# Kernel tuning notes

Measured on AMD Instinct MI355X. Metric: run time of the kernel, lower is better.

The kernel has to match this reference:

```python
import jax, jax.numpy as jnp
import numpy as np

B, T, M, E, H, D = 4, 1024, 1024, 1024, 16, 64
SCALE = D ** (-0.5)


def setup_inputs() -> dict:
    key = jax.random.key(0)
    ks = jax.random.split(key, 8)
    w = 0.02  # weight scale for numerical stability of softmax
    return {
        "x": jax.random.normal(ks[0], (B, T, E), jnp.float32),
        "xl_memory": jax.random.normal(ks[1], (B, M, 2, H * D), jnp.float32),
        "relative_positions": jax.random.normal(ks[2], (H, T, M + T), jnp.float32),
        "Wq": jax.random.normal(ks[3], (E, H * D), jnp.float32) * w,
        "bq": jnp.zeros((H * D,), jnp.float32),
        "Wk": jax.random.normal(ks[4], (E, H * D), jnp.float32) * w,
        "bk": jnp.zeros((H * D,), jnp.float32),
        "Wv": jax.random.normal(ks[5], (E, H * D), jnp.float32) * w,
        "bv": jnp.zeros((H * D,), jnp.float32),
        "Wo": jax.random.normal(ks[6], (H * D, E), jnp.float32) * w,
        "bo": jnp.zeros((E,), jnp.float32),
    }


def reference(x, xl_memory, relative_positions, Wq, bq, Wk, bk, Wv, bv, Wo, bo):
    b, t, _ = x.shape
    q = (x @ Wq + bq) * SCALE                     # [b, t, H*D] (scale applied to queries)
    k = x @ Wk + bk
    v = x @ Wv + bv
    k_xl = xl_memory[:, :, 0]                      # [b, m, H*D]
    v_xl = xl_memory[:, :, 1]
    m = k_xl.shape[1]
    keys = jnp.concatenate((k_xl, k), axis=1)      # [b, j, H*D], j = m + t
    values = jnp.concatenate((v_xl, v), axis=1)
    j = keys.shape[1]

    qh = q.reshape(b, t, H, D).transpose(0, 2, 1, 3)       # b h i d
    kh = keys.reshape(b, j, H, D).transpose(0, 2, 1, 3)    # b h j d
    vh = values.reshape(b, j, H, D).transpose(0, 2, 1, 3)  # b h j d

    qk = jnp.einsum("bhid,bhjd->bhij", qh, kh)
    qk = relative_positions[..., -t:, -j:] + qk
    qk = qk * SCALE                                # second scale, faithful to source
    mask = jnp.triu(jnp.ones((t, j), dtype=bool), j - t + 1)
    qk = jnp.where(mask, -jnp.inf, qk)
    attn = jax.nn.softmax(qk, axis=-1)             # dropout p=0.0 -> identity

    qkv = jnp.einsum("bhij,bhjd->bhid", attn, vh)
    qkv = qkv.transpose(0, 2, 1, 3).reshape(b, t, H * D)
    out = qkv @ Wo + bo

    kv_memories = jnp.stack((keys, values), axis=-2)  # [b, j, 2, H*D]
    kv_to_add_xl = kv_memories[:, -m:]                 # [b, m, 2, H*D]
    return out, kv_to_add_xl
```

## Files before the change

### kernel.cpp

```cpp
#include <hip/hip_runtime.h>
#include <hip/hip_bf16.h>

typedef unsigned short u16;
typedef unsigned int u32;
typedef __attribute__((ext_vector_type(8))) short short8;
typedef __attribute__((ext_vector_type(4))) float f32x4;

#define B_ 4
#define T_ 1024
#define E_ 1024
#define NH 16
#define HD 1024
#define JTOT 2048
#define SCALE 0.125f
#define LOG2E 1.44269504f

__device__ __forceinline__ u16 f2b(float f) {
  u32 x = __float_as_uint(f);
  u32 r = (x + 0x7fffu + ((x >> 16) & 1u)) >> 16;
  return (u16)r;
}
__device__ __forceinline__ u16 f2b_fast(float f) {
  return (u16)((__float_as_uint(f) + 0x8000u) >> 16);
}
__device__ __forceinline__ float b2f(u16 b) {
  return __uint_as_float((u32)b << 16);
}
__device__ __forceinline__ float fexp2(float x) {
  float r;
  asm("v_exp_f32 %0, %1" : "=v"(r) : "v"(x));
  return r;
}

__device__ __forceinline__ void gload_lds16(const void* g, void* l) {
  __builtin_amdgcn_global_load_lds((const __attribute__((address_space(1))) u32*)g,
                                   (__attribute__((address_space(3))) u32*)l, 16, 0, 0);
}

__device__ __forceinline__ short8 pack8(float4 f0, float4 f1) {
  short8 o;
  o[0] = (short)f2b(f0.x); o[1] = (short)f2b(f0.y);
  o[2] = (short)f2b(f0.z); o[3] = (short)f2b(f0.w);
  o[4] = (short)f2b(f1.x); o[5] = (short)f2b(f1.y);
  o[6] = (short)f2b(f1.z); o[7] = (short)f2b(f1.w);
  return o;
}

__global__ __launch_bounds__(256) void cvt_bf16(const float* __restrict__ in,
                                                u16* __restrict__ out, int n8) {
  int i = blockIdx.x * 256 + threadIdx.x;
  if (i >= n8) return;
  const float4* p = (const float4*)in + (size_t)i * 2;
  ((short8*)out)[i] = pack8(p[0], p[1]);
}

__global__ __launch_bounds__(256) void cvt_w4T(const float* __restrict__ Wq, const float* __restrict__ Wk,
                                               const float* __restrict__ Wv, const float* __restrict__ Wo,
                                               u16* __restrict__ wqkvT, u16* __restrict__ woT) {
  __shared__ float tile[64][65];
  const float* W;
  u16* WT;
  int z = blockIdx.z;
  if (z == 0) { W = Wq; WT = wqkvT; }
  else if (z == 1) { W = Wk; WT = wqkvT + (size_t)1024 * 1024; }
  else if (z == 2) { W = Wv; WT = wqkvT + (size_t)2048 * 1024; }
  else { W = Wo; WT = woT; }
  int t = threadIdx.x;
  int r0 = blockIdx.y * 64, c0 = blockIdx.x * 64;
#pragma unroll
  for (int i = 0; i < 16; ++i) {
    int r = i * 4 + (t >> 6), c = t & 63;
    tile[r][c] = W[(size_t)(r0 + r) * 1024 + c0 + c];
  }
  __syncthreads();
#pragma unroll
  for (int i = 0; i < 16; ++i) {
    int r = i * 4 + (t >> 6), c = t & 63;
    WT[(size_t)(c0 + r) * 1024 + r0 + c] = f2b(tile[c][r]);
  }
}

__global__ __launch_bounds__(256) void cvt_xl_k(const float* __restrict__ xl, u16* __restrict__ kt) {
  int i = blockIdx.x * 256 + threadIdx.x;
  int hd8 = i & 127, j = (i >> 7) & 1023, b = i >> 17;
  const float4* p = (const float4*)(xl + ((((size_t)b * 1024 + j) * 2 + 0) * 1024 + (size_t)hd8 * 8));
  short8 o = pack8(p[0], p[1]);
  int h = hd8 >> 3, d0 = (hd8 & 7) * 8;
  int jc = j >> 6, jl = j & 63;
  u16* dst = kt + (((size_t)(b * 16 + h) * 32 + jc) * 4096) + jl * 64 + (d0 ^ (((jl >> 2) & 3) << 4));
  *(short8*)dst = o;
}

__global__ __launch_bounds__(256) void cvt_xl_vT(const float* __restrict__ xl, u16* __restrict__ vt) {
  __shared__ u16 Vl[64 * 72];
  int bx = blockIdx.x;
  int jc = bx & 15, h = (bx >> 4) & 15, b = bx >> 8;
  int t = threadIdx.x;
  int j0 = jc * 64;
#pragma unroll
  for (int it = 0; it < 2; ++it) {
    int p = t + 256 * it;
    int j = p >> 3, d8 = p & 7;
    const float4* src = (const float4*)(xl + ((((size_t)b * 1024 + j0 + j) * 2 + 1) * 1024 + h * 64 + (size_t)d8 * 8));
    *(short8*)&Vl[j * 72 + d8 * 8] = pack8(src[0], src[1]);
  }
  __syncthreads();
#pragma unroll
  for (int it = 0; it < 2; ++it) {
    int p = t + 256 * it;
    int d = p >> 3, j8 = p & 7;
    short8 o;
#pragma unroll
    for (int e = 0; e < 8; ++e) o[e] = (short)Vl[(j8 * 8 + e) * 72 + d];
    u16* dst = vt + (((size_t)(b * 16 + h) * 32 + jc) * 4096) + d * 64 + ((j8 * 8) ^ (((d >> 2) & 3) << 4));
    *(short8*)dst = o;
  }
}

__global__ __launch_bounds__(256) void trans_vnew(const u16* __restrict__ vb, u16* __restrict__ vt) {
  __shared__ u16 Vl[64 * 72];
  int bx = blockIdx.x;
  int jcl = bx & 15, h = (bx >> 4) & 15, b = bx >> 8;
  int jc = 16 + jcl;
  int t = threadIdx.x;
  int t0 = jcl * 64;
#pragma unroll
  for (int it = 0; it < 2; ++it) {
    int p = t + 256 * it;
    int j = p >> 3, d8 = p & 7;
    *(short8*)&Vl[j * 72 + d8 * 8] =
        *(const short8*)&vb[((size_t)b * 1024 + t0 + j) * 1024 + h * 64 + d8 * 8];
  }
  __syncthreads();
#pragma unroll
  for (int it = 0; it < 2; ++it) {
    int p = t + 256 * it;
    int d = p >> 3, j8 = p & 7;
    short8 o;
#pragma unroll
    for (int e = 0; e < 8; ++e) o[e] = (short)Vl[(j8 * 8 + e) * 72 + d];
    u16* dst = vt + (((size_t)(b * 16 + h) * 32 + jc) * 4096) + d * 64 + ((j8 * 8) ^ (((d >> 2) & 3) << 4));
    *(short8*)dst = o;
  }
}

__global__ __launch_bounds__(256) void gemm_qkv(
    const u16* __restrict__ A, const u16* __restrict__ BT,
    const float* __restrict__ b0, const float* __restrict__ b1, const float* __restrict__ b2,
    u16* __restrict__ qb, u16* __restrict__ kbp, u16* __restrict__ kt, u16* __restrict__ vb) {
  __shared__ __align__(16) u16 As[128 * 32];
  __shared__ __align__(16) u16 Bs[128 * 32];
  const int t = threadIdx.x;
  const int lane = t & 63, wv = t >> 6;
  const int wr = wv >> 1, wc = wv & 1;
  const int m0 = (blockIdx.x / 24) * 128;
  const int n0 = (blockIdx.x % 24) * 128;
  const int lr = lane & 15, lg = lane >> 4;

  f32x4 acc[4][4] = {};

  for (int kc = 0; kc < 1024; kc += 32) {
    __syncthreads();
#pragma unroll
    for (int i = 0; i < 2; ++i) {
      int p = t + 256 * i;
      gload_lds16(A + (size_t)(m0 + (p >> 2)) * 1024 + kc + (p & 3) * 8, &As[p * 8]);
    }
#pragma unroll
    for (int i = 0; i < 2; ++i) {
      int p = t + 256 * i;
      gload_lds16(BT + (size_t)(n0 + (p >> 2)) * 1024 + kc + (p & 3) * 8, &Bs[p * 8]);
    }
    __syncthreads();

    short8 af[4], bf[4];
#pragma unroll
    for (int mf = 0; mf < 4; ++mf)
      af[mf] = *(const short8*)&As[(wr * 64 + mf * 16 + lr) * 32 + lg * 8];
#pragma unroll
    for (int nf = 0; nf < 4; ++nf)
      bf[nf] = *(const short8*)&Bs[(wc * 64 + nf * 16 + lr) * 32 + lg * 8];
#pragma unroll
    for (int mf = 0; mf < 4; ++mf)
#pragma unroll
      for (int nf = 0; nf < 4; ++nf)
        acc[mf][nf] = __builtin_amdgcn_mfma_f32_16x16x32_bf16(af[mf], bf[nf], acc[mf][nf], 0, 0, 0);
  }

#pragma unroll
  for (int mf = 0; mf < 4; ++mf) {
#pragma unroll
    for (int nf = 0; nf < 4; ++nf) {
#pragma unroll
      for (int r = 0; r < 4; ++r) {
        int row = m0 + wr * 64 + mf * 16 + lg * 4 + r;
        int col = n0 + wc * 64 + nf * 16 + lr;
        float v = acc[mf][nf][r];
        int b = row >> 10, tt = row & 1023;
        if (col < 1024) {
          v += b0[col];
          qb[(size_t)row * HD + col] = f2b(v * (SCALE * SCALE * LOG2E));
        } else if (col < 2048) {
          int hd = col - 1024;
          u16 kv16 = f2b(v + b1[hd]);
          kbp[(size_t)(b * 1024 + tt) * 1024 + hd] = kv16;
          int h = hd >> 6, d = hd & 63, jl = tt & 63, jc = 16 + (tt >> 6);
          kt[(((size_t)(b * 16 + h) * 32 + jc) * 4096) + jl * 64 + (d ^ (((jl >> 2) & 3) << 4))] = kv16;
        } else {
          int hd = col - 2048;
          vb[(size_t)(b * 1024 + tt) * 1024 + hd] = f2b(v + b2[hd]);
        }
      }
    }
  }
}

__global__ __launch_bounds__(256) void kv_expand(const u16* __restrict__ kbp, const u16* __restrict__ vbp,
                                                 float* __restrict__ kvout) {
  int i = blockIdx.x * 256 + threadIdx.x;
  int hd8 = i & 127, tt = (i >> 7) & 1023, b = i >> 17;
  size_t src = ((size_t)(b * 1024 + tt)) * 1024 + (size_t)hd8 * 8;
  short8 k8 = *(const short8*)&kbp[src];
  short8 v8 = *(const short8*)&vbp[src];
  float4 k0, k1, v0, v1;
#pragma unroll
  for (int e = 0; e < 4; ++e) {
    ((float*)&k0)[e] = b2f((u16)k8[e]); ((float*)&k1)[e] = b2f((u16)k8[e + 4]);
    ((float*)&v0)[e] = b2f((u16)v8[e]); ((float*)&v1)[e] = b2f((u16)v8[e + 4]);
  }
  float* kdst = kvout + (((size_t)(b * 1024 + tt) * 2 + 0) * 1024) + hd8 * 8;
  float* vdst = kvout + (((size_t)(b * 1024 + tt) * 2 + 1) * 1024) + hd8 * 8;
  ((float4*)kdst)[0] = k0; ((float4*)kdst)[1] = k1;
  ((float4*)vdst)[0] = v0; ((float4*)vdst)[1] = v1;
}

__global__ __launch_bounds__(256) void gemm_out(
    const u16* __restrict__ A, const u16* __restrict__ BT,
    const float* __restrict__ bias, float* __restrict__ outf) {
  __shared__ __align__(16) u16 As[64 * 32];
  __shared__ __align__(16) u16 Bs[128 * 32];
  const int t = threadIdx.x;
  const int lane = t & 63, wv = t >> 6;
  const int wr = wv >> 1, wc = wv & 1;
  const int m0 = (blockIdx.x >> 3) * 64;
  const int n0 = (blockIdx.x & 7) * 128;
  const int lr = lane & 15, lg = lane >> 4;

  f32x4 acc[2][4] = {};

  for (int kc = 0; kc < 1024; kc += 32) {
    __syncthreads();
    gload_lds16(A + (size_t)(m0 + (t >> 2)) * 1024 + kc + (t & 3) * 8, &As[t * 8]);
#pragma unroll
    for (int i = 0; i < 2; ++i) {
      int p = t + 256 * i;
      gload_lds16(BT + (size_t)(n0 + (p >> 2)) * 1024 + kc + (p & 3) * 8, &Bs[p * 8]);
    }
    __syncthreads();

    short8 af[2], bf[4];
#pragma unroll
    for (int mf = 0; mf < 2; ++mf)
      af[mf] = *(const short8*)&As[(wr * 32 + mf * 16 + lr) * 32 + lg * 8];
#pragma unroll
    for (int nf = 0; nf < 4; ++nf)
      bf[nf] = *(const short8*)&Bs[(wc * 64 + nf * 16 + lr) * 32 + lg * 8];
#pragma unroll
    for (int mf = 0; mf < 2; ++mf)
#pragma unroll
      for (int nf = 0; nf < 4; ++nf)
        acc[mf][nf] = __builtin_amdgcn_mfma_f32_16x16x32_bf16(af[mf], bf[nf], acc[mf][nf], 0, 0, 0);
  }

#pragma unroll
  for (int mf = 0; mf < 2; ++mf)
#pragma unroll
    for (int nf = 0; nf < 4; ++nf)
#pragma unroll
      for (int r = 0; r < 4; ++r) {
        int row = m0 + wr * 32 + mf * 16 + lg * 4 + r;
        int col = n0 + wc * 64 + nf * 16 + lr;
        outf[(size_t)row * E_ + col] = acc[mf][nf][r] + bias[col];
      }
}

__global__ __launch_bounds__(256) void attn_kernel(
    const u16* __restrict__ qb, const u16* __restrict__ kt, const u16* __restrict__ vt,
    const float* __restrict__ rel, u16* __restrict__ aout) {
  __shared__ __align__(16) u16 Ks[2][4096];
  __shared__ __align__(16) u16 Vs[2][4096];
  __shared__ __align__(16) u16 Pl[4096];
  const int bx = blockIdx.x;
  const int b = bx & 3, h = (bx >> 2) & 15, qt = bx >> 6;
  const int i0 = qt * 64;
  const int t = threadIdx.x, lane = t & 63, w = t >> 6;
  const int lr = lane & 15, lg = lane >> 4;
  const int sel = (lr >> 2) & 3;
  const float RC = SCALE * LOG2E;

  const u16* ktb = kt + (size_t)(b * 16 + h) * 32 * 4096;
  const u16* vtb = vt + (size_t)(b * 16 + h) * 32 * 4096;
  const float* relbase = rel + (size_t)h * T_ * JTOT;
  const int ib = i0 + w * 16 + lg * 4;

  short8 qf[2];
#pragma unroll
  for (int kc = 0; kc < 2; ++kc)
    qf[kc] = *(const short8*)&qb[(size_t)(b * T_ + i0 + w * 16 + lr) * HD + h * 64 + kc * 32 + lg * 8];

  short8 vf5;
#pragma unroll
  for (int e = 0; e < 8; ++e) vf5[e] = (lr == 0) ? (short)0x3f80 : (short)0;

  const int nch = qt + 17;

  auto stage = [&](int buf, int jc2) {
    const u16* ksrc = ktb + (size_t)jc2 * 4096;
    const u16* vsrc = vtb + (size_t)jc2 * 4096;
    gload_lds16(ksrc + t * 8, &Ks[buf][t * 8]);
    gload_lds16(ksrc + (t + 256) * 8, &Ks[buf][(t + 256) * 8]);
    gload_lds16(vsrc + t * 8, &Vs[buf][t * 8]);
    gload_lds16(vsrc + (t + 256) * 8, &Vs[buf][(t + 256) * 8]);
  };

  float rl[4][4];
  auto loadrel = [&](int j0) {
#pragma unroll
    for (int nf = 0; nf < 4; ++nf)
#pragma unroll
      for (int r = 0; r < 4; ++r)
        rl[nf][r] = relbase[(size_t)(ib + r) * JTOT + j0 + nf * 16 + lr];
  };

  stage(0, 0);
  asm volatile("" ::: "memory");
  loadrel(0);

  f32x4 o[5] = {};
  float mrow[4];
#pragma unroll
  for (int r = 0; r < 4; ++r) mrow[r] = -__builtin_inff();

  int cur = 0;
  for (int jc = 0; jc < nch; ++jc) {
    asm volatile("s_waitcnt vmcnt(16)" ::: "memory");
    __builtin_amdgcn_sched_barrier(0);
    asm volatile("s_barrier" ::: "memory");
    if (jc + 1 < nch) stage(cur ^ 1, jc + 1);
    asm volatile("" ::: "memory");

    f32x4 s4[4] = {};
    __builtin_amdgcn_s_setprio(1);
#pragma unroll
    for (int nf = 0; nf < 4; ++nf)
#pragma unroll
      for (int kc = 0; kc < 2; ++kc) {
        short8 kf = *(const short8*)&Ks[cur][(nf * 16 + lr) * 64 + ((kc * 32 + lg * 8) ^ (sel << 4))];
        s4[nf] = __builtin_amdgcn_mfma_f32_16x16x32_bf16(qf[kc], kf, s4[nf], 0, 0, 0);
      }
    __builtin_amdgcn_s_setprio(0);

    float p[4][4], lmax[4];
    const bool domask = (jc == qt + 16);
#pragma unroll
    for (int nf = 0; nf < 4; ++nf)
#pragma unroll
      for (int r = 0; r < 4; ++r) {
        float v = fmaf(rl[nf][r], RC, s4[nf][r]);
        if (domask && (nf * 16 + lr) > (w * 16 + lg * 4 + r)) v = -__builtin_inff();
        p[nf][r] = v;
      }
#pragma unroll
    for (int r = 0; r < 4; ++r)
      lmax[r] = fmaxf(fmaxf(p[0][r], p[1][r]), fmaxf(p[2][r], p[3][r]));
    if (jc + 1 < nch) loadrel((jc + 1) * 64);

    float need = -__builtin_inff();
#pragma unroll
    for (int r = 0; r < 4; ++r) need = fmaxf(need, lmax[r] - mrow[r]);
    const bool dores = !__all(need <= 11.0f);
    if (dores) {
      float chmax[4], sc[4];
#pragma unroll
      for (int r = 0; r < 4; ++r) chmax[r] = lmax[r];
#pragma unroll
      for (int msk = 1; msk <= 8; msk <<= 1)
#pragma unroll
        for (int r = 0; r < 4; ++r)
          chmax[r] = fmaxf(chmax[r], __shfl_xor(chmax[r], msk, 64));
#pragma unroll
      for (int r = 0; r < 4; ++r) {
        float nm = fmaxf(mrow[r], chmax[r]);
        sc[r] = fexp2(mrow[r] - nm);
        mrow[r] = nm;
      }
#pragma unroll
      for (int nf = 0; nf < 5; ++nf)
#pragma unroll
        for (int r = 0; r < 4; ++r) o[nf][r] *= sc[r];
    }

#pragma unroll
    for (int nf = 0; nf < 4; ++nf)
#pragma unroll
      for (int r = 0; r < 4; ++r) {
        float pe = fexp2(p[nf][r] - mrow[r]);
        Pl[(w * 16 + lg * 4 + r) * 64 + (((nf ^ lg) << 4) + lr)] = f2b_fast(pe);
      }

    __builtin_amdgcn_s_setprio(1);
#pragma unroll
    for (int kc = 0; kc < 2; ++kc) {
      const int pcol = (kc * 32 + lg * 8) ^ (sel << 4);
      short8 pa = *(const short8*)&Pl[(w * 16 + lr) * 64 + pcol];
#pragma unroll
      for (int nf = 0; nf < 4; ++nf) {
        short8 vf = *(const short8*)&Vs[cur][(nf * 16 + lr) * 64 + pcol];
        o[nf] = __builtin_amdgcn_mfma_f32_16x16x32_bf16(pa, vf, o[nf], 0, 0, 0);
      }
      o[4] = __builtin_amdgcn_mfma_f32_16x16x32_bf16(pa, vf5, o[4], 0, 0, 0);
    }
    __builtin_amdgcn_s_setprio(0);
    asm volatile("" ::: "memory");
    cur ^= 1;
  }

  float inv[4];
#pragma unroll
  for (int r = 0; r < 4; ++r)
    inv[r] = 1.0f / __shfl(o[4][r], lane & 48, 64);
#pragma unroll
  for (int nf = 0; nf < 4; ++nf)
#pragma unroll
    for (int r = 0; r < 4; ++r) {
      int i = i0 + w * 16 + lg * 4 + r, d = nf * 16 + lr;
      aout[(size_t)(b * T_ + i) * HD + h * 64 + d] = f2b_fast(o[nf][r] * inv[r]);
    }
}

extern "C" void kernel_launch(void* const* d_in, const int* in_sizes, int n_in,
                              void* d_out, int out_size, void* d_ws, size_t ws_size,
                              hipStream_t stream) {
  const float* x  = (const float*)d_in[0];
  const float* xl = (const float*)d_in[1];
  const float* rel = (const float*)d_in[2];
  const float* Wq = (const float*)d_in[3];
  const float* bq = (const float*)d_in[4];
  const float* Wk = (const float*)d_in[5];
  const float* bk = (const float*)d_in[6];
  const float* Wv = (const float*)d_in[7];
  const float* bv = (const float*)d_in[8];
  const float* Wo = (const float*)d_in[9];
  const float* bo = (const float*)d_in[10];

  float* out = (float*)d_out;
  float* kvout = out + (size_t)B_ * T_ * E_;

  char* ws = (char*)d_ws;
  u16* xb    = (u16*)ws; ws += (size_t)4096 * 1024 * 2;
  u16* wqkvT = (u16*)ws; ws += (size_t)3072 * 1024 * 2;
  u16* woT   = (u16*)ws; ws += (size_t)1024 * 1024 * 2;
  u16* qbuf  = (u16*)ws; ws += (size_t)4096 * 1024 * 2;
  u16* kt    = (u16*)ws; ws += (size_t)B_ * NH * 32 * 4096 * 2;
  u16* vt    = (u16*)ws; ws += (size_t)B_ * NH * 32 * 4096 * 2;
  u16* vbn   = (u16*)ws; ws += (size_t)4096 * 1024 * 2;
  u16* kbp   = (u16*)ws; ws += (size_t)4096 * 1024 * 2;
  u16* aout  = (u16*)ws; ws += (size_t)4096 * 1024 * 2;

  cvt_bf16<<<2048, 256, 0, stream>>>(x, xb, 524288);
  cvt_w4T<<<dim3(16, 16, 4), 256, 0, stream>>>(Wq, Wk, Wv, Wo, wqkvT, woT);
  cvt_xl_k<<<2048, 256, 0, stream>>>(xl, kt);
  cvt_xl_vT<<<1024, 256, 0, stream>>>(xl, vt);

  gemm_qkv<<<32 * 24, 256, 0, stream>>>(xb, wqkvT, bq, bk, bv, qbuf, kbp, kt, vbn);
  kv_expand<<<2048, 256, 0, stream>>>(kbp, vbn, kvout);
  trans_vnew<<<1024, 256, 0, stream>>>(vbn, vt);
  attn_kernel<<<1024, 256, 0, stream>>>(qbuf, kt, vt, rel, aout);
  gemm_out<<<512, 256, 0, stream>>>(aout, woT, bo, out);
}
```

Baseline: 219.6 us.

## Double attention query tile to 128 rows with reordered causal tiles and new swizzle

The attention kernel now handles 128 query rows per block instead of 64, with each wave computing two 16-row fragments. This halves how often each K/V chunk is loaded per query and reuses each K/V fragment read from LDS across two MFMAs. Query tiles are issued in a paired order that mixes long and short causal tiles to balance work, and the K/V LDS swizzle changes to an 8-way XOR pattern in every producer kernel. In exchange the kernel needs more registers and LDS (the P buffer doubles), only 512 blocks are launched, and more relative-position values are held in flight.

```diff
diff --git a/kernel.cpp b/kernel.cpp
--- a/kernel.cpp
+++ b/kernel.cpp
@@ -87,7 +87,7 @@
   short8 o = pack8(p[0], p[1]);
   int h = hd8 >> 3, d0 = (hd8 & 7) * 8;
   int jc = j >> 6, jl = j & 63;
-  u16* dst = kt + (((size_t)(b * 16 + h) * 32 + jc) * 4096) + jl * 64 + (d0 ^ (((jl >> 2) & 3) << 4));
+  u16* dst = kt + (((size_t)(b * 16 + h) * 32 + jc) * 4096) + jl * 64 + (d0 ^ ((jl & 7) << 3));
   *(short8*)dst = o;
 }
 
@@ -112,7 +112,7 @@
     short8 o;
 #pragma unroll
     for (int e = 0; e < 8; ++e) o[e] = (short)Vl[(j8 * 8 + e) * 72 + d];
-    u16* dst = vt + (((size_t)(b * 16 + h) * 32 + jc) * 4096) + d * 64 + ((j8 * 8) ^ (((d >> 2) & 3) << 4));
+    u16* dst = vt + (((size_t)(b * 16 + h) * 32 + jc) * 4096) + d * 64 + ((j8 * 8) ^ ((d & 7) << 3));
     *(short8*)dst = o;
   }
 }
@@ -139,7 +139,7 @@
     short8 o;
 #pragma unroll
     for (int e = 0; e < 8; ++e) o[e] = (short)Vl[(j8 * 8 + e) * 72 + d];
-    u16* dst = vt + (((size_t)(b * 16 + h) * 32 + jc) * 4096) + d * 64 + ((j8 * 8) ^ (((d >> 2) & 3) << 4));
+    u16* dst = vt + (((size_t)(b * 16 + h) * 32 + jc) * 4096) + d * 64 + ((j8 * 8) ^ ((d & 7) << 3));
     *(short8*)dst = o;
   }
 }
@@ -205,7 +205,7 @@
           u16 kv16 = f2b(v + b1[hd]);
           kbp[(size_t)(b * 1024 + tt) * 1024 + hd] = kv16;
           int h = hd >> 6, d = hd & 63, jl = tt & 63, jc = 16 + (tt >> 6);
-          kt[(((size_t)(b * 16 + h) * 32 + jc) * 4096) + jl * 64 + (d ^ (((jl >> 2) & 3) << 4))] = kv16;
+          kt[(((size_t)(b * 16 + h) * 32 + jc) * 4096) + jl * 64 + (d ^ ((jl & 7) << 3))] = kv16;
         } else {
           int hd = col - 2048;
           vb[(size_t)(b * 1024 + tt) * 1024 + hd] = f2b(v + b2[hd]);
@@ -289,30 +289,34 @@
     const float* __restrict__ rel, u16* __restrict__ aout) {
   __shared__ __align__(16) u16 Ks[2][4096];
   __shared__ __align__(16) u16 Vs[2][4096];
-  __shared__ __align__(16) u16 Pl[4096];
+  __shared__ __align__(16) u16 Pl[8192];
   const int bx = blockIdx.x;
-  const int b = bx & 3, h = (bx >> 2) & 15, qt = bx >> 6;
-  const int i0 = qt * 64;
+  const int b = bx & 3, h = (bx >> 2) & 15;
+  const int q_ = bx >> 6;
+  const int qt = q_ < 4 ? q_ : 11 - q_;
+  const int i0 = qt * 128;
   const int t = threadIdx.x, lane = t & 63, w = t >> 6;
   const int lr = lane & 15, lg = lane >> 4;
-  const int sel = (lr >> 2) & 3;
+  const int swz = (lr & 7) << 3;
+  const int psw = ((lr >> 2) & 3) << 4;
   const float RC = SCALE * LOG2E;
 
   const u16* ktb = kt + (size_t)(b * 16 + h) * 32 * 4096;
   const u16* vtb = vt + (size_t)(b * 16 + h) * 32 * 4096;
   const float* relbase = rel + (size_t)h * T_ * JTOT;
-  const int ib = i0 + w * 16 + lg * 4;
-
-  short8 qf[2];
-#pragma unroll
-  for (int kc = 0; kc < 2; ++kc)
-    qf[kc] = *(const short8*)&qb[(size_t)(b * T_ + i0 + w * 16 + lr) * HD + h * 64 + kc * 32 + lg * 8];
+
+  short8 qf[2][2];
+#pragma unroll
+  for (int mf = 0; mf < 2; ++mf)
+#pragma unroll
+    for (int kc = 0; kc < 2; ++kc)
+      qf[mf][kc] = *(const short8*)&qb[(size_t)(b * T_ + i0 + w * 32 + mf * 16 + lr) * HD + h * 64 + kc * 32 + lg * 8];
 
   short8 vf5;
 #pragma unroll
   for (int e = 0; e < 8; ++e) vf5[e] = (lr == 0) ? (short)0x3f80 : (short)0;
 
-  const int nch = qt + 17;
+  const int nch = qt * 2 + 18;
 
   auto stage = [&](int buf, int jc2) {
     const u16* ksrc = ktb + (size_t)jc2 * 4096;
@@ -323,119 +327,148 @@
     gload_lds16(vsrc + (t + 256) * 8, &Vs[buf][(t + 256) * 8]);
   };
 
-  float rl[4][4];
+  float rl[2][4][4];
   auto loadrel = [&](int j0) {
 #pragma unroll
-    for (int nf = 0; nf < 4; ++nf)
-#pragma unroll
-      for (int r = 0; r < 4; ++r)
-        rl[nf][r] = relbase[(size_t)(ib + r) * JTOT + j0 + nf * 16 + lr];
+    for (int mf = 0; mf < 2; ++mf) {
+      const float* rb = relbase + (size_t)(i0 + w * 32 + mf * 16 + lg * 4) * JTOT + j0;
+#pragma unroll
+      for (int nf = 0; nf < 4; ++nf)
+#pragma unroll
+        for (int r = 0; r < 4; ++r)
+          rl[mf][nf][r] = rb[(size_t)r * JTOT + nf * 16 + lr];
+    }
   };
 
   stage(0, 0);
-  asm volatile("" ::: "memory");
+  __builtin_amdgcn_sched_barrier(0);
   loadrel(0);
 
-  f32x4 o[5] = {};
-  float mrow[4];
-#pragma unroll
-  for (int r = 0; r < 4; ++r) mrow[r] = -__builtin_inff();
+  f32x4 o[2][4] = {};
+  f32x4 o5[2] = {};
+  float mrow[2][4];
+#pragma unroll
+  for (int mf = 0; mf < 2; ++mf)
+#pragma unroll
+    for (int r = 0; r < 4; ++r) mrow[mf][r] = -__builtin_inff();
 
   int cur = 0;
   for (int jc = 0; jc < nch; ++jc) {
-    asm volatile("s_waitcnt vmcnt(16)" ::: "memory");
+    asm volatile("s_waitcnt vmcnt(32)" ::: "memory");
     __builtin_amdgcn_sched_barrier(0);
     asm volatile("s_barrier" ::: "memory");
     if (jc + 1 < nch) stage(cur ^ 1, jc + 1);
-    asm volatile("" ::: "memory");
-
-    f32x4 s4[4] = {};
+    __builtin_amdgcn_sched_barrier(0);
+
+    f32x4 s4[2][4] = {};
     __builtin_amdgcn_s_setprio(1);
 #pragma unroll
     for (int nf = 0; nf < 4; ++nf)
 #pragma unroll
       for (int kc = 0; kc < 2; ++kc) {
-        short8 kf = *(const short8*)&Ks[cur][(nf * 16 + lr) * 64 + ((kc * 32 + lg * 8) ^ (sel << 4))];
-        s4[nf] = __builtin_amdgcn_mfma_f32_16x16x32_bf16(qf[kc], kf, s4[nf], 0, 0, 0);
+        short8 kf = *(const short8*)&Ks[cur][(nf * 16 + lr) * 64 + ((kc * 32 + lg * 8) ^ swz)];
+#pragma unroll
+        for (int mf = 0; mf < 2; ++mf)
+          s4[mf][nf] = __builtin_amdgcn_mfma_f32_16x16x32_bf16(qf[mf][kc], kf, s4[mf][nf], 0, 0, 0);
       }
     __builtin_amdgcn_s_setprio(0);
 
-    float p[4][4], lmax[4];
-    const bool domask = (jc == qt + 16);
-#pragma unroll
-    for (int nf = 0; nf < 4; ++nf)
-#pragma unroll
-      for (int r = 0; r < 4; ++r) {
-        float v = fmaf(rl[nf][r], RC, s4[nf][r]);
-        if (domask && (nf * 16 + lr) > (w * 16 + lg * 4 + r)) v = -__builtin_inff();
-        p[nf][r] = v;
-      }
-#pragma unroll
-    for (int r = 0; r < 4; ++r)
-      lmax[r] = fmaxf(fmaxf(p[0][r], p[1][r]), fmaxf(p[2][r], p[3][r]));
+    float p[2][4][4], lmax[2][4];
+    const bool domask = (jc >= nch - 2);
+#pragma unroll
+    for (int mf = 0; mf < 2; ++mf) {
+      const int ibm = i0 + w * 32 + mf * 16 + lg * 4 + 1024 - jc * 64;
+#pragma unroll
+      for (int nf = 0; nf < 4; ++nf)
+#pragma unroll
+        for (int r = 0; r < 4; ++r) {
+          float v = fmaf(rl[mf][nf][r], RC, s4[mf][nf][r]);
+          if (domask && (nf * 16 + lr) > (ibm + r)) v = -__builtin_inff();
+          p[mf][nf][r] = v;
+        }
+#pragma unroll
+      for (int r = 0; r < 4; ++r)
+        lmax[mf][r] = fmaxf(fmaxf(p[mf][0][r], p[mf][1][r]), fmaxf(p[mf][2][r], p[mf][3][r]));
+    }
     if (jc + 1 < nch) loadrel((jc + 1) * 64);
 
     float need = -__builtin_inff();
 #pragma unroll
-    for (int r = 0; r < 4; ++r) need = fmaxf(need, lmax[r] - mrow[r]);
+    for (int mf = 0; mf < 2; ++mf)
+#pragma unroll
+      for (int r = 0; r < 4; ++r) need = fmaxf(need, lmax[mf][r] - mrow[mf][r]);
     const bool dores = !__all(need <= 11.0f);
     if (dores) {
-      float chmax[4], sc[4];
-#pragma unroll
-      for (int r = 0; r < 4; ++r) chmax[r] = lmax[r];
-#pragma unroll
-      for (int msk = 1; msk <= 8; msk <<= 1)
-#pragma unroll
-        for (int r = 0; r < 4; ++r)
-          chmax[r] = fmaxf(chmax[r], __shfl_xor(chmax[r], msk, 64));
-#pragma unroll
-      for (int r = 0; r < 4; ++r) {
-        float nm = fmaxf(mrow[r], chmax[r]);
-        sc[r] = fexp2(mrow[r] - nm);
-        mrow[r] = nm;
+#pragma unroll
+      for (int mf = 0; mf < 2; ++mf) {
+        float chmax[4], sc[4];
+#pragma unroll
+        for (int r = 0; r < 4; ++r) chmax[r] = lmax[mf][r];
+#pragma unroll
+        for (int msk = 1; msk <= 8; msk <<= 1)
+#pragma unroll
+          for (int r = 0; r < 4; ++r)
+            chmax[r] = fmaxf(chmax[r], __shfl_xor(chmax[r], msk, 64));
+#pragma unroll
+        for (int r = 0; r < 4; ++r) {
+          float nm = fmaxf(mrow[mf][r], chmax[r]);
+          sc[r] = fexp2(mrow[mf][r] - nm);
+          mrow[mf][r] = nm;
+        }
+#pragma unroll
+        for (int nf = 0; nf < 4; ++nf)
+#pragma unroll
+          for (int r = 0; r < 4; ++r) o[mf][nf][r] *= sc[r];
+#pragma unroll
+        for (int r = 0; r < 4; ++r) o5[mf][r] *= sc[r];
       }
-#pragma unroll
-      for (int nf = 0; nf < 5; ++nf)
-#pragma unroll
-        for (int r = 0; r < 4; ++r) o[nf][r] *= sc[r];
-    }
-
-#pragma unroll
-    for (int nf = 0; nf < 4; ++nf)
-#pragma unroll
-      for (int r = 0; r < 4; ++r) {
-        float pe = fexp2(p[nf][r] - mrow[r]);
-        Pl[(w * 16 + lg * 4 + r) * 64 + (((nf ^ lg) << 4) + lr)] = f2b_fast(pe);
+    }
+
+#pragma unroll
+    for (int mf = 0; mf < 2; ++mf)
+#pragma unroll
+      for (int nf = 0; nf < 4; ++nf)
+#pragma unroll
+        for (int r = 0; r < 4; ++r) {
+          float pe = fexp2(p[mf][nf][r] - mrow[mf][r]);
+          Pl[(w * 32 + mf * 16 + lg * 4 + r) * 64 + (((nf ^ lg) << 4) + lr)] = f2b_fast(pe);
+        }
+
+    __builtin_amdgcn_s_setprio(1);
+#pragma unroll
+    for (int kc = 0; kc < 2; ++kc) {
+      short8 vf[4];
+#pragma unroll
+      for (int nf = 0; nf < 4; ++nf)
+        vf[nf] = *(const short8*)&Vs[cur][(nf * 16 + lr) * 64 + ((kc * 32 + lg * 8) ^ swz)];
+#pragma unroll
+      for (int mf = 0; mf < 2; ++mf) {
+        short8 pa = *(const short8*)&Pl[(w * 32 + mf * 16 + lr) * 64 + ((kc * 32 + lg * 8) ^ psw)];
+#pragma unroll
+        for (int nf = 0; nf < 4; ++nf)
+          o[mf][nf] = __builtin_amdgcn_mfma_f32_16x16x32_bf16(pa, vf[nf], o[mf][nf], 0, 0, 0);
+        o5[mf] = __builtin_amdgcn_mfma_f32_16x16x32_bf16(pa, vf5, o5[mf], 0, 0, 0);
       }
-
-    __builtin_amdgcn_s_setprio(1);
-#pragma unroll
-    for (int kc = 0; kc < 2; ++kc) {
-      const int pcol = (kc * 32 + lg * 8) ^ (sel << 4);
-      short8 pa = *(const short8*)&Pl[(w * 16 + lr) * 64 + pcol];
-#pragma unroll
-      for (int nf = 0; nf < 4; ++nf) {
-        short8 vf = *(const short8*)&Vs[cur][(nf * 16 + lr) * 64 + pcol];
-        o[nf] = __builtin_amdgcn_mfma_f32_16x16x32_bf16(pa, vf, o[nf], 0, 0, 0);
-      }
-      o[4] = __builtin_amdgcn_mfma_f32_16x16x32_bf16(pa, vf5, o[4], 0, 0, 0);
     }
     __builtin_amdgcn_s_setprio(0);
     asm volatile("" ::: "memory");
     cur ^= 1;
   }
 
-  float inv[4];
-#pragma unroll
-  for (int r = 0; r < 4; ++r)
-    inv[r] = 1.0f / __shfl(o[4][r], lane & 48, 64);
-#pragma unroll
-  for (int nf = 0; nf < 4; ++nf)
-#pragma unroll
-    for (int r = 0; r < 4; ++r) {
-      int i = i0 + w * 16 + lg * 4 + r, d = nf * 16 + lr;
-      aout[(size_t)(b * T_ + i) * HD + h * 64 + d] = f2b_fast(o[nf][r] * inv[r]);
-    }
+#pragma unroll
+  for (int mf = 0; mf < 2; ++mf) {
+    float inv[4];
+#pragma unroll
+    for (int r = 0; r < 4; ++r)
+      inv[r] = 1.0f / __shfl(o5[mf][r], lane & 48, 64);
+#pragma unroll
+    for (int nf = 0; nf < 4; ++nf)
+#pragma unroll
+      for (int r = 0; r < 4; ++r) {
+        int i = i0 + w * 32 + mf * 16 + lg * 4 + r, d = nf * 16 + lr;
+        aout[(size_t)(b * T_ + i) * HD + h * 64 + d] = f2b_fast(o[mf][nf][r] * inv[r]);
+      }
+  }
 }
 
 extern "C" void kernel_launch(void* const* d_in, const int* in_sizes, int n_in,
@@ -475,6 +508,6 @@
   gemm_qkv<<<32 * 24, 256, 0, stream>>>(xb, wqkvT, bq, bk, bv, qbuf, kbp, kt, vbn);
   kv_expand<<<2048, 256, 0, stream>>>(kbp, vbn, kvout);
   trans_vnew<<<1024, 256, 0, stream>>>(vbn, vt);
-  attn_kernel<<<1024, 256, 0, stream>>>(qbuf, kt, vt, rel, aout);
+  attn_kernel<<<512, 256, 0, stream>>>(qbuf, kt, vt, rel, aout);
   gemm_out<<<512, 256, 0, stream>>>(aout, woT, bo, out);
 }
```

Measured after the change: 256.0 us. 1.17x slower.

## Change K/V LDS swizzle, double-buffer rel prefetch two chunks ahead, add occupancy bound

Applied to the files above, without the earlier changes.

Changes the XOR swizzle for the K and V tiles from a 4-row group pattern to a per-row 8-element pattern. The change is made in every producer kernel and in the attention-side reads, to reduce LDS bank conflicts on the short8 reads. The relative-position bias is now prefetched two chunks ahead using two register buffers, with the loop unrolled by two, so global-load latency is better hidden. Adds a launch-bounds occupancy hint of 4 blocks, which risks register pressure or spills given the extra rel buffer.

```diff
diff --git a/kernel.cpp b/kernel.cpp
--- a/kernel.cpp
+++ b/kernel.cpp
@@ -87,7 +87,7 @@
   short8 o = pack8(p[0], p[1]);
   int h = hd8 >> 3, d0 = (hd8 & 7) * 8;
   int jc = j >> 6, jl = j & 63;
-  u16* dst = kt + (((size_t)(b * 16 + h) * 32 + jc) * 4096) + jl * 64 + (d0 ^ (((jl >> 2) & 3) << 4));
+  u16* dst = kt + (((size_t)(b * 16 + h) * 32 + jc) * 4096) + jl * 64 + (d0 ^ ((jl & 7) << 3));
   *(short8*)dst = o;
 }
 
@@ -112,7 +112,7 @@
     short8 o;
 #pragma unroll
     for (int e = 0; e < 8; ++e) o[e] = (short)Vl[(j8 * 8 + e) * 72 + d];
-    u16* dst = vt + (((size_t)(b * 16 + h) * 32 + jc) * 4096) + d * 64 + ((j8 * 8) ^ (((d >> 2) & 3) << 4));
+    u16* dst = vt + (((size_t)(b * 16 + h) * 32 + jc) * 4096) + d * 64 + ((j8 * 8) ^ ((d & 7) << 3));
     *(short8*)dst = o;
   }
 }
@@ -139,7 +139,7 @@
     short8 o;
 #pragma unroll
     for (int e = 0; e < 8; ++e) o[e] = (short)Vl[(j8 * 8 + e) * 72 + d];
-    u16* dst = vt + (((size_t)(b * 16 + h) * 32 + jc) * 4096) + d * 64 + ((j8 * 8) ^ (((d >> 2) & 3) << 4));
+    u16* dst = vt + (((size_t)(b * 16 + h) * 32 + jc) * 4096) + d * 64 + ((j8 * 8) ^ ((d & 7) << 3));
     *(short8*)dst = o;
   }
 }
@@ -205,7 +205,7 @@
           u16 kv16 = f2b(v + b1[hd]);
           kbp[(size_t)(b * 1024 + tt) * 1024 + hd] = kv16;
           int h = hd >> 6, d = hd & 63, jl = tt & 63, jc = 16 + (tt >> 6);
-          kt[(((size_t)(b * 16 + h) * 32 + jc) * 4096) + jl * 64 + (d ^ (((jl >> 2) & 3) << 4))] = kv16;
+          kt[(((size_t)(b * 16 + h) * 32 + jc) * 4096) + jl * 64 + (d ^ ((jl & 7) << 3))] = kv16;
         } else {
           int hd = col - 2048;
           vb[(size_t)(b * 1024 + tt) * 1024 + hd] = f2b(v + b2[hd]);
@@ -284,7 +284,7 @@
       }
 }
 
-__global__ __launch_bounds__(256) void attn_kernel(
+__global__ __launch_bounds__(256, 4) void attn_kernel(
     const u16* __restrict__ qb, const u16* __restrict__ kt, const u16* __restrict__ vt,
     const float* __restrict__ rel, u16* __restrict__ aout) {
   __shared__ __align__(16) u16 Ks[2][4096];
@@ -295,7 +295,8 @@
   const int i0 = qt * 64;
   const int t = threadIdx.x, lane = t & 63, w = t >> 6;
   const int lr = lane & 15, lg = lane >> 4;
-  const int sel = (lr >> 2) & 3;
+  const int swz = (lr & 7) << 3;
+  const int psw = ((lr >> 2) & 3) << 4;
   const float RC = SCALE * LOG2E;
 
   const u16* ktb = kt + (size_t)(b * 16 + h) * 32 * 4096;
@@ -323,18 +324,19 @@
     gload_lds16(vsrc + (t + 256) * 8, &Vs[buf][(t + 256) * 8]);
   };
 
-  float rl[4][4];
-  auto loadrel = [&](int j0) {
+  auto loadrel = [&](int j0, float (&rlf)[4][4]) {
 #pragma unroll
     for (int nf = 0; nf < 4; ++nf)
 #pragma unroll
       for (int r = 0; r < 4; ++r)
-        rl[nf][r] = relbase[(size_t)(ib + r) * JTOT + j0 + nf * 16 + lr];
+        rlf[nf][r] = relbase[(size_t)(ib + r) * JTOT + j0 + nf * 16 + lr];
   };
 
+  float rlA[4][4], rlB[4][4];
   stage(0, 0);
-  asm volatile("" ::: "memory");
-  loadrel(0);
+  __builtin_amdgcn_sched_barrier(0);
+  loadrel(0, rlA);
+  loadrel(64, rlB);
 
   f32x4 o[5] = {};
   float mrow[4];
@@ -342,12 +344,12 @@
   for (int r = 0; r < 4; ++r) mrow[r] = -__builtin_inff();
 
   int cur = 0;
-  for (int jc = 0; jc < nch; ++jc) {
+  auto chunkfn = [&](int jc, float (&rlu)[4][4]) {
     asm volatile("s_waitcnt vmcnt(16)" ::: "memory");
     __builtin_amdgcn_sched_barrier(0);
     asm volatile("s_barrier" ::: "memory");
     if (jc + 1 < nch) stage(cur ^ 1, jc + 1);
-    asm volatile("" ::: "memory");
+    __builtin_amdgcn_sched_barrier(0);
 
     f32x4 s4[4] = {};
     __builtin_amdgcn_s_setprio(1);
@@ -355,7 +357,7 @@
     for (int nf = 0; nf < 4; ++nf)
 #pragma unroll
       for (int kc = 0; kc < 2; ++kc) {
-        short8 kf = *(const short8*)&Ks[cur][(nf * 16 + lr) * 64 + ((kc * 32 + lg * 8) ^ (sel << 4))];
+        short8 kf = *(const short8*)&Ks[cur][(nf * 16 + lr) * 64 + ((kc * 32 + lg * 8) ^ swz)];
         s4[nf] = __builtin_amdgcn_mfma_f32_16x16x32_bf16(qf[kc], kf, s4[nf], 0, 0, 0);
       }
     __builtin_amdgcn_s_setprio(0);
@@ -366,14 +368,14 @@
     for (int nf = 0; nf < 4; ++nf)
 #pragma unroll
       for (int r = 0; r < 4; ++r) {
-        float v = fmaf(rl[nf][r], RC, s4[nf][r]);
+        float v = fmaf(rlu[nf][r], RC, s4[nf][r]);
         if (domask && (nf * 16 + lr) > (w * 16 + lg * 4 + r)) v = -__builtin_inff();
         p[nf][r] = v;
       }
+    if (jc + 2 < nch) loadrel((jc + 2) * 64, rlu);
 #pragma unroll
     for (int r = 0; r < 4; ++r)
       lmax[r] = fmaxf(fmaxf(p[0][r], p[1][r]), fmaxf(p[2][r], p[3][r]));
-    if (jc + 1 < nch) loadrel((jc + 1) * 64);
 
     float need = -__builtin_inff();
 #pragma unroll
@@ -411,19 +413,25 @@
     __builtin_amdgcn_s_setprio(1);
 #pragma unroll
     for (int kc = 0; kc < 2; ++kc) {
-      const int pcol = (kc * 32 + lg * 8) ^ (sel << 4);
-      short8 pa = *(const short8*)&Pl[(w * 16 + lr) * 64 + pcol];
+      const int pcol = kc * 32 + lg * 8;
+      short8 pa = *(const short8*)&Pl[(w * 16 + lr) * 64 + (pcol ^ psw)];
 #pragma unroll
       for (int nf = 0; nf < 4; ++nf) {
-        short8 vf = *(const short8*)&Vs[cur][(nf * 16 + lr) * 64 + pcol];
+        short8 vf = *(const short8*)&Vs[cur][(nf * 16 + lr) * 64 + (pcol ^ swz)];
         o[nf] = __builtin_amdgcn_mfma_f32_16x16x32_bf16(pa, vf, o[nf], 0, 0, 0);
       }
       o[4] = __builtin_amdgcn_mfma_f32_16x16x32_bf16(pa, vf5, o[4], 0, 0, 0);
     }
     __builtin_amdgcn_s_setprio(0);
-    asm volatile("" ::: "memory");
     cur ^= 1;
-  }
+  };
+
+  int jc = 0;
+  for (; jc + 1 < nch; jc += 2) {
+    chunkfn(jc, rlA);
+    chunkfn(jc + 1, rlB);
+  }
+  if (jc < nch) chunkfn(jc, rlA);
 
   float inv[4];
 #pragma unroll
```

Measured after the change: 226.4 us. 3.1% more time.
